# Performance work log

Hardware: AMD Instinct MI355X
Metric: run time of the kernel (lower is better)

## Reference

```python
import jax, jax.numpy as jnp
import numpy as np
import math

SEQLEN, DIM, N_HEADS = 2048, 4096, 32
HEAD_DIM = DIM // N_HEADS
NEG_INF = -1e30  # exp underflows to exactly 0, same effect as -inf without NaN risk


def setup_inputs() -> dict:
    key = jax.random.key(0)
    ks = jax.random.split(key, 7)
    scale = 1.0 / math.sqrt(DIM)
    x = jax.random.normal(ks[0], (SEQLEN, DIM), dtype=jnp.float32)
    weight_q = jax.random.normal(ks[1], (DIM, DIM), dtype=jnp.float32) * scale
    weight_k = jax.random.normal(ks[2], (DIM, DIM), dtype=jnp.float32) * scale
    weight_v = jax.random.normal(ks[3], (DIM, DIM), dtype=jnp.float32) * scale
    weight_o = jax.random.normal(ks[4], (DIM, DIM), dtype=jnp.float32) * scale
    # RoPE frequencies: freqs_cis = exp(i * t * theta_j), standard LLaMA schedule
    inv_freq = 1.0 / (10000.0 ** (np.arange(0, HEAD_DIM, 2, dtype=np.float32) / HEAD_DIM))
    angles = np.arange(SEQLEN, dtype=np.float32)[:, None] * inv_freq[None, :]  # [S, hd/2]
    freqs_cos = jnp.asarray(np.cos(angles), dtype=jnp.float32)
    freqs_sin = jnp.asarray(np.sin(angles), dtype=jnp.float32)
    # additive causal mask [S, S]
    mask = jnp.where(jnp.triu(jnp.ones((SEQLEN, SEQLEN), dtype=bool), k=1), NEG_INF, 0.0).astype(jnp.float32)
    return {"x": x, "weight_q": weight_q, "weight_k": weight_k, "weight_v": weight_v,
            "weight_o": weight_o, "freqs_cos": freqs_cos, "freqs_sin": freqs_sin,
            "mask": mask, "start_pos": 0}


def _apply_rope(t, cos, sin):
    # t: [S, H, hd]; cos/sin: [S, hd/2]
    tr = t.reshape(*t.shape[:-1], -1, 2)           # [S, H, hd/2, 2]
    t_re, t_im = tr[..., 0], tr[..., 1]
    c = cos[:, None, :]
    s = sin[:, None, :]
    out_re = t_re * c - t_im * s
    out_im = t_re * s + t_im * c
    return jnp.stack([out_re, out_im], axis=-1).reshape(t.shape)


def reference(x, weight_q, weight_k, weight_v, weight_o, freqs_cos, freqs_sin, mask, start_pos):
    S, D = x.shape
    hd = freqs_cos.shape[-1] * 2
    H = D // hd
    # the per-head double loop over wq[j][i] is exactly a full [D,D] projection
    xq = (x @ weight_q).reshape(S, H, hd)
    xk = (x @ weight_k).reshape(S, H, hd)
    xv = (x @ weight_v).reshape(S, H, hd)
    xq = _apply_rope(xq, freqs_cos, freqs_sin)
    xk = _apply_rope(xk, freqs_cos, freqs_sin)
    # start_pos == 0 prefill: cache slice == freshly computed keys/values
    scores = jnp.einsum('shd,thd->hst', xq, xk) / jnp.sqrt(jnp.float32(hd))
    scores = scores + mask[None, :, :]
    probs = jax.nn.softmax(scores.astype(jnp.float32), axis=-1).astype(xq.dtype)
    qkv = jnp.einsum('hst,thd->shd', probs, xv).reshape(S, D)
    return qkv @ weight_o
```

## Files before the change

### kernel.cpp

```cpp
#include <hip/hip_runtime.h>
#include <hip/hip_bf16.h>
#include <type_traits>

typedef __hip_bfloat16 bf16;
typedef __attribute__((ext_vector_type(8))) short s8v;
typedef __attribute__((ext_vector_type(4))) short s4v;
typedef __attribute__((ext_vector_type(4))) float f4v;

#define MFMA16(A, B, C) __builtin_amdgcn_mfma_f32_16x16x32_bf16((A), (B), (C), 0, 0, 0)

constexpr int SEQ = 2048;
constexpr int DIM = 4096;
constexpr int NH  = 32;
constexpr int HD  = 128;

__device__ __forceinline__ short f2bs(float f) {
    __hip_bfloat16_raw r = __float2bfloat16(f);
    return (short)r.x;
}

__device__ __forceinline__ void ld_g2l(const bf16* g, bf16* l) {
    __builtin_amdgcn_global_load_lds(
        (const __attribute__((address_space(1))) void*)g,
        (__attribute__((address_space(3))) void*)l, 16, 0, 0);
}

__global__ void convert_bf16(const float* __restrict__ s, bf16* __restrict__ d) {
    int i = blockIdx.x * blockDim.x + threadIdx.x;
    float4 f = ((const float4*)s)[i];
    s4v o;
    o[0] = f2bs(f.x); o[1] = f2bs(f.y); o[2] = f2bs(f.z); o[3] = f2bs(f.w);
    *(s4v*)(d + (size_t)i * 4) = o;
}

__global__ __launch_bounds__(256) void convt_bf16(const float* __restrict__ src,
                                                  bf16* __restrict__ dst,
                                                  int R, int C) {
    __shared__ float t[64][65];
    const int c0 = blockIdx.x * 64, r0 = blockIdx.y * 64;
    const int tid = threadIdx.x;
    const int lr = tid >> 4;
    const int lc = (tid & 15) * 4;
#pragma unroll
    for (int i = 0; i < 4; i++) {
        float4 f = *(const float4*)(src + (size_t)(r0 + lr + 16 * i) * C + c0 + lc);
        t[lr + 16 * i][lc]     = f.x;
        t[lr + 16 * i][lc + 1] = f.y;
        t[lr + 16 * i][lc + 2] = f.z;
        t[lr + 16 * i][lc + 3] = f.w;
    }
    __syncthreads();
    const int oc = tid >> 2;
#pragma unroll
    for (int i = 0; i < 2; i++) {
        int rr = (tid & 3) * 8 + 32 * i;
        s8v o;
#pragma unroll
        for (int e = 0; e < 8; e++) o[e] = f2bs(t[rr + e][oc]);
        *(s8v*)(dst + (size_t)(c0 + oc) * R + r0 + rr) = o;
    }
}

template <typename CT>
__global__ __launch_bounds__(512, 2) void gemm_8p(const bf16* __restrict__ A,
                                                  const bf16* __restrict__ Bt,
                                                  CT* __restrict__ C,
                                                  int M, int N, int K) {
    __shared__ bf16 As_[2][128 * 64];
    __shared__ bf16 Bs_[2][256 * 64];
    const int tid  = threadIdx.x;
    const int lane = tid & 63;
    const int wv   = tid >> 6;
    const int m16  = lane & 15;
    const int quad = lane >> 4;
    const int wm   = wv >> 2, wn = wv & 3;

    const int v   = (int)(blockIdx.y * gridDim.x + blockIdx.x);
    const int s_  = v >> 3;
    const int bn  = (v & 7) * 2 + (s_ >> 4);
    const int bm  = s_ & 15;

    const bf16* Ab = A  + (size_t)bm * 128 * K;
    const bf16* Bb = Bt + (size_t)bn * 256 * K;

    const int i0   = wv * 64 + lane;
    const int row0 = i0 >> 3;
    const int gc8  = ((i0 & 7) ^ (row0 & 7)) * 8;
    const int dst0 = (wv * 64) * 8;
    const int dst1 = (512 + wv * 64) * 8;

    const int aB = (wm * 64 + m16) * 64;
    const int bB = (wn * 64 + m16) * 64;
    const int swz = m16 & 7;
    const int c0k = ((0 + quad) ^ swz) * 8;
    const int c1k = ((4 + quad) ^ swz) * 8;

    const int NT = K >> 6;

    f4v acc[4][4] = {};
    s8v aR[4][2], bR[4][2];

#define STAGEU(gb, lb) do { \
        ld_g2l((gb) + (size_t)row0 * K + gc8, (lb) + dst0); \
        ld_g2l((gb) + (size_t)(row0 + 64) * K + gc8, (lb) + dst1); } while (0)
#define LDA_(i, ks) aR[i][ks] = *(const s8v*)(Ac + aB + (i) * 1024 + ((ks) ? c1k : c0k))
#define LDB_(j, ks) bR[j][ks] = *(const s8v*)(Bc + bB + (j) * 1024 + ((ks) ? c1k : c0k))
#define MMQ(i, j) do { acc[i][j] = MFMA16(aR[i][0], bR[j][0], acc[i][j]); \
                       acc[i][j] = MFMA16(aR[i][1], bR[j][1], acc[i][j]); } while (0)
#define BARX()  __builtin_amdgcn_s_barrier()
#define LGKM0() do { asm volatile("s_waitcnt lgkmcnt(0)" ::: "memory"); \
                     __builtin_amdgcn_sched_barrier(0); } while (0)

    STAGEU(Ab, As_[0]);
    STAGEU(Bb, Bs_[0]);
    STAGEU(Bb + (size_t)128 * K, Bs_[0] + 128 * 64);
    if (NT > 1) {
        STAGEU(Bb + 64, Bs_[1]);
        STAGEU(Bb + (size_t)128 * K + 64, Bs_[1] + 128 * 64);
        STAGEU(Ab + 64, As_[1]);
        asm volatile("s_waitcnt vmcnt(6)" ::: "memory");
    } else {
        asm volatile("s_waitcnt vmcnt(0)" ::: "memory");
    }
    __builtin_amdgcn_sched_barrier(0);
    BARX();

    for (int t = 0; t < NT; ++t) {
        const int cur = t & 1;
        const bf16* Ac = As_[cur];
        const bf16* Bc = Bs_[cur];
        const bool more = (t + 2 < NT);
        const int k2 = (t + 2) << 6;

        LDA_(0, 0); LDA_(0, 1); LDA_(1, 0); LDA_(1, 1);
        LDB_(0, 0); LDB_(0, 1); LDB_(1, 0); LDB_(1, 1);
        BARX(); LGKM0();
        __builtin_amdgcn_s_setprio(1);
        MMQ(0, 0); MMQ(0, 1); MMQ(1, 0); MMQ(1, 1);
        __builtin_amdgcn_s_setprio(0);
        BARX();

        LDB_(2, 0); LDB_(2, 1); LDB_(3, 0); LDB_(3, 1);
        BARX(); LGKM0();
        __builtin_amdgcn_s_setprio(1);
        MMQ(0, 2); MMQ(0, 3); MMQ(1, 2); MMQ(1, 3);
        __builtin_amdgcn_s_setprio(0);
        BARX();

        LDA_(2, 0); LDA_(2, 1); LDA_(3, 0); LDA_(3, 1);
        if (more) {
            STAGEU(Bb + k2, Bs_[cur]);
            STAGEU(Bb + (size_t)128 * K + k2, Bs_[cur] + 128 * 64);
        }
        BARX(); LGKM0();
        __builtin_amdgcn_s_setprio(1);
        MMQ(2, 0); MMQ(2, 1); MMQ(3, 0); MMQ(3, 1);
        __builtin_amdgcn_s_setprio(0);
        BARX();

        if (more) {
            STAGEU(Ab + k2, As_[cur]);
            asm volatile("s_waitcnt vmcnt(6)" ::: "memory");
        } else {
            asm volatile("s_waitcnt vmcnt(0)" ::: "memory");
        }
        __builtin_amdgcn_sched_barrier(0);
        BARX();
        __builtin_amdgcn_s_setprio(1);
        MMQ(2, 2); MMQ(2, 3); MMQ(3, 2); MMQ(3, 3);
        __builtin_amdgcn_s_setprio(0);
        BARX();
    }

#undef STAGEU
#undef LDA_
#undef LDB_
#undef MMQ
#undef BARX
#undef LGKM0

#pragma unroll
    for (int i = 0; i < 4; i++)
#pragma unroll
        for (int j = 0; j < 4; j++)
#pragma unroll
            for (int r = 0; r < 4; r++) {
                int row = bm * 128 + wm * 64 + i * 16 + quad * 4 + r;
                int col = bn * 256 + wn * 64 + j * 16 + m16;
                if constexpr (std::is_same<CT, float>::value)
                    C[(size_t)row * N + col] = acc[i][j][r];
                else
                    C[(size_t)row * N + col] = __float2bfloat16(acc[i][j][r]);
            }
}

template <typename AT, typename CT>
__global__ __launch_bounds__(256) void gemm_nat(const AT* __restrict__ A,
                                                const float* __restrict__ B,
                                                CT* __restrict__ C,
                                                int M, int N, int K) {
    __shared__ short As[128][40];
    __shared__ short Bs[128][40];
    const int tid  = threadIdx.x;
    const int lane = tid & 63;
    const int w    = tid >> 6;
    const int m16  = lane & 15;
    const int quad = lane >> 4;
    const int wm   = w >> 1, wn = w & 1;
    const int bm   = blockIdx.y, bn = blockIdx.x;

    const AT* Ab = A + (size_t)bm * 128 * K;

    f4v acc[4][4] = {};
    const int r0 = tid >> 2;
    const int kc = (tid & 3) * 8;

    for (int k0 = 0; k0 < K; k0 += 32) {
        if constexpr (std::is_same<AT, float>::value) {
#pragma unroll
            for (int half = 0; half < 2; half++) {
                const float* src = Ab + (size_t)(r0 + 64 * half) * K + k0 + kc;
                float4 f0 = *(const float4*)(src);
                float4 f1 = *(const float4*)(src + 4);
                s8v t;
                t[0] = f2bs(f0.x); t[1] = f2bs(f0.y); t[2] = f2bs(f0.z); t[3] = f2bs(f0.w);
                t[4] = f2bs(f1.x); t[5] = f2bs(f1.y); t[6] = f2bs(f1.z); t[7] = f2bs(f1.w);
                *(s8v*)&As[r0 + 64 * half][kc] = t;
            }
        } else {
            *(s8v*)&As[r0][kc]      = *(const s8v*)(Ab + (size_t)r0 * K + k0 + kc);
            *(s8v*)&As[r0 + 64][kc] = *(const s8v*)(Ab + (size_t)(r0 + 64) * K + k0 + kc);
        }
#pragma unroll
        for (int v = tid; v < 512; v += 256) {
            int kr = v >> 4;
            int nc = (v & 15) * 8;
            const float* src = B + (size_t)(k0 + kr) * N + bn * 128 + nc;
            float4 f0 = *(const float4*)(src);
            float4 f1 = *(const float4*)(src + 4);
            Bs[nc + 0][kr] = f2bs(f0.x); Bs[nc + 1][kr] = f2bs(f0.y);
            Bs[nc + 2][kr] = f2bs(f0.z); Bs[nc + 3][kr] = f2bs(f0.w);
            Bs[nc + 4][kr] = f2bs(f1.x); Bs[nc + 5][kr] = f2bs(f1.y);
            Bs[nc + 6][kr] = f2bs(f1.z); Bs[nc + 7][kr] = f2bs(f1.w);
        }
        __syncthreads();

        s8v a[4], b[4];
#pragma unroll
        for (int i = 0; i < 4; i++) a[i] = *(s8v*)&As[wm * 64 + i * 16 + m16][quad * 8];
#pragma unroll
        for (int j = 0; j < 4; j++) b[j] = *(s8v*)&Bs[wn * 64 + j * 16 + m16][quad * 8];
#pragma unroll
        for (int i = 0; i < 4; i++)
#pragma unroll
            for (int j = 0; j < 4; j++) acc[i][j] = MFMA16(a[i], b[j], acc[i][j]);
        __syncthreads();
    }

#pragma unroll
    for (int i = 0; i < 4; i++)
#pragma unroll
        for (int j = 0; j < 4; j++)
#pragma unroll
            for (int r = 0; r < 4; r++) {
                int row = bm * 128 + wm * 64 + i * 16 + quad * 4 + r;
                int col = bn * 128 + wn * 64 + j * 16 + m16;
                if constexpr (std::is_same<CT, float>::value)
                    C[(size_t)row * N + col] = acc[i][j][r];
                else
                    C[(size_t)row * N + col] = __float2bfloat16(acc[i][j][r]);
            }
}

__global__ void rope_kernel(bf16* __restrict__ Q, bf16* __restrict__ K,
                            const float* __restrict__ fc, const float* __restrict__ fs) {
    int tid = blockIdx.x * blockDim.x + threadIdx.x;
    int s = tid >> 11;
    int r = tid & 2047;
    int i = r & 63;
    float c  = fc[s * 64 + i];
    float sn = fs[s * 64 + i];
    size_t idx = (size_t)s * DIM + 2 * r;
    float qre = __bfloat162float(Q[idx]), qim = __bfloat162float(Q[idx + 1]);
    Q[idx]     = __float2bfloat16(qre * c - qim * sn);
    Q[idx + 1] = __float2bfloat16(qre * sn + qim * c);
    float kre = __bfloat162float(K[idx]), kim = __bfloat162float(K[idx + 1]);
    K[idx]     = __float2bfloat16(kre * c - kim * sn);
    K[idx + 1] = __float2bfloat16(kre * sn + kim * c);
}

__global__ __launch_bounds__(256) void attn_kernel(const bf16* __restrict__ Q,
                                                   const bf16* __restrict__ K,
                                                   const bf16* __restrict__ V,
                                                   bf16* __restrict__ O) {
    __shared__ short Ks[64][136];
    __shared__ short Vs[128][72];
    __shared__ short Ps[64][72];

    const int p  = blockIdx.x;
    const int h  = blockIdx.y;
    const int tid  = threadIdx.x;
    const int w    = tid >> 6;
    const int lane = tid & 63;
    const int m16  = lane & 15;
    const int quad = lane >> 4;
    const float scale = 0.08838834764831845f;
    const int NQB = (int)gridDim.x * 2;

    const int rn  = tid >> 4;
    const int rc  = (tid & 15) * 8;
    const int dcs = (tid & 15) & 7;

    for (int half = 0; half < 2; half++) {
        const int qb = half ? (NQB - 1 - p) : p;

        s8v aq[4];
        {
            const bf16* qp = Q + (size_t)(qb * 64 + w * 16 + m16) * DIM + h * HD + quad * 8;
#pragma unroll
            for (int ks = 0; ks < 4; ks++) aq[ks] = *(const s8v*)(qp + ks * 32);
        }

        f4v acc[8] = {};
        float mrow[4] = {-1e30f, -1e30f, -1e30f, -1e30f};
        float lrow[4] = {};

        s8v kreg[4], vreg[4];
        {
            const bf16* kp = K + (size_t)rn * DIM + h * HD + rc;
            const bf16* vp = V + (size_t)rn * DIM + h * HD + rc;
#pragma unroll
            for (int it = 0; it < 4; it++) {
                kreg[it] = *(const s8v*)(kp + (size_t)it * 16 * DIM);
                vreg[it] = *(const s8v*)(vp + (size_t)it * 16 * DIM);
            }
        }

        for (int kt = 0; kt <= qb; kt++) {
#pragma unroll
            for (int it = 0; it < 4; it++)
                *(s8v*)&Ks[it * 16 + rn][rc] = kreg[it];
#pragma unroll
            for (int it = 0; it < 4; it++) {
                int n   = it * 16 + rn;
                int col = (((n >> 3) ^ dcs) << 3) | (n & 7);
#pragma unroll
                for (int e = 0; e < 8; e++) Vs[rc + e][col] = vreg[it][e];
            }
            __syncthreads();

            if (kt < qb) {
                const bf16* kp = K + (size_t)((kt + 1) * 64 + rn) * DIM + h * HD + rc;
                const bf16* vp = V + (size_t)((kt + 1) * 64 + rn) * DIM + h * HD + rc;
#pragma unroll
                for (int it = 0; it < 4; it++) {
                    kreg[it] = *(const s8v*)(kp + (size_t)it * 16 * DIM);
                    vreg[it] = *(const s8v*)(vp + (size_t)it * 16 * DIM);
                }
            }

            f4v sc[4] = {};
#pragma unroll
            for (int j = 0; j < 4; j++)
#pragma unroll
                for (int ks = 0; ks < 4; ks++) {
                    s8v bk = *(s8v*)&Ks[j * 16 + m16][ks * 32 + quad * 8];
                    sc[j] = MFMA16(aq[ks], bk, sc[j]);
                }

            const bool diag = (kt == qb);
#pragma unroll
            for (int j = 0; j < 4; j++)
#pragma unroll
                for (int r = 0; r < 4; r++) {
                    float sv = sc[j][r] * scale;
                    if (diag && (j * 16 + m16) > (w * 16 + quad * 4 + r)) sv = -1e30f;
                    sc[j][r] = sv;
                }

#pragma unroll
            for (int r = 0; r < 4; r++) {
                float mx = fmaxf(fmaxf(sc[0][r], sc[1][r]), fmaxf(sc[2][r], sc[3][r]));
#pragma unroll
                for (int off = 1; off < 16; off <<= 1) mx = fmaxf(mx, __shfl_xor(mx, off, 64));
                float mn    = fmaxf(mrow[r], mx);
                float alpha = __expf(mrow[r] - mn);
                mrow[r] = mn;
                float rs = 0.f;
#pragma unroll
                for (int j = 0; j < 4; j++) {
                    float pj = __expf(sc[j][r] - mn);
                    sc[j][r] = pj;
                    rs += pj;
                }
#pragma unroll
                for (int off = 1; off < 16; off <<= 1) rs += __shfl_xor(rs, off, 64);
                lrow[r] = lrow[r] * alpha + rs;
#pragma unroll
                for (int jo = 0; jo < 8; jo++) acc[jo][r] = acc[jo][r] * alpha;
            }

#pragma unroll
            for (int j = 0; j < 4; j++)
#pragma unroll
                for (int r = 0; r < 4; r++)
                    Ps[w * 16 + quad * 4 + r][j * 16 + m16] = f2bs(sc[j][r]);
            asm volatile("s_waitcnt lgkmcnt(0)" ::: "memory");
            __builtin_amdgcn_sched_barrier(0);

#pragma unroll
            for (int ks2 = 0; ks2 < 2; ks2++) {
                s8v ap = *(s8v*)&Ps[w * 16 + m16][ks2 * 32 + quad * 8];
#pragma unroll
                for (int jo = 0; jo < 8; jo++) {
                    int dv = jo * 16 + m16;
                    int cg = (((ks2 * 4 + quad) ^ ((dv >> 3) & 7)) << 3);
                    s8v bv = *(s8v*)&Vs[dv][cg];
                    acc[jo] = MFMA16(ap, bv, acc[jo]);
                }
            }
            __syncthreads();
        }

#pragma unroll
        for (int jo = 0; jo < 8; jo++)
#pragma unroll
            for (int r = 0; r < 4; r++) {
                float o = acc[jo][r] / fmaxf(lrow[r], 1e-30f);
                int row = qb * 64 + w * 16 + quad * 4 + r;
                int col = h * HD + jo * 16 + m16;
                O[(size_t)row * DIM + col] = __float2bfloat16(o);
            }
    }
}

extern "C" void kernel_launch(void* const* d_in, const int* in_sizes, int n_in,
                              void* d_out, int out_size, void* d_ws, size_t ws_size,
                              hipStream_t stream) {
    const float* x  = (const float*)d_in[0];
    const float* wq = (const float*)d_in[1];
    const float* wk = (const float*)d_in[2];
    const float* wv = (const float*)d_in[3];
    const float* wo = (const float*)d_in[4];
    const float* fc = (const float*)d_in[5];
    const float* fs = (const float*)d_in[6];

    float* out = (float*)d_out;

    const size_t SZ = (size_t)SEQ * DIM;
    const size_t WZ = (size_t)DIM * DIM;
    bf16* Q  = (bf16*)d_ws;
    bf16* Kb = Q + SZ;
    bf16* V  = Kb + SZ;
    bf16* AO = V + SZ;

    const size_t need = (5 * SZ + WZ) * sizeof(bf16);

    if (ws_size >= need) {
        bf16* xb = AO + SZ;
        bf16* wb = xb + SZ;

        dim3 tGw(DIM / 64, DIM / 64);
        dim3 gG8(DIM / 256, SEQ / 128);

        convert_bf16<<<(int)(SZ / 4 / 256), 256, 0, stream>>>(x, xb);

        convt_bf16<<<tGw, 256, 0, stream>>>(wq, wb, DIM, DIM);
        gemm_8p<bf16><<<gG8, 512, 0, stream>>>(xb, wb, Q, SEQ, DIM, DIM);
        convt_bf16<<<tGw, 256, 0, stream>>>(wk, wb, DIM, DIM);
        gemm_8p<bf16><<<gG8, 512, 0, stream>>>(xb, wb, Kb, SEQ, DIM, DIM);
        convt_bf16<<<tGw, 256, 0, stream>>>(wv, wb, DIM, DIM);
        gemm_8p<bf16><<<gG8, 512, 0, stream>>>(xb, wb, V, SEQ, DIM, DIM);

        rope_kernel<<<(SEQ * (DIM / 2)) / 256, 256, 0, stream>>>(Q, Kb, fc, fs);
        attn_kernel<<<dim3(SEQ / 128, NH), 256, 0, stream>>>(Q, Kb, V, AO);

        convt_bf16<<<tGw, 256, 0, stream>>>(wo, wb, DIM, DIM);
        gemm_8p<float><<<gG8, 512, 0, stream>>>(AO, wb, out, SEQ, DIM, DIM);
    } else {
        dim3 gGn(DIM / 128, SEQ / 128);
        gemm_nat<float, bf16><<<gGn, 256, 0, stream>>>(x, wq, Q,  SEQ, DIM, DIM);
        gemm_nat<float, bf16><<<gGn, 256, 0, stream>>>(x, wk, Kb, SEQ, DIM, DIM);
        gemm_nat<float, bf16><<<gGn, 256, 0, stream>>>(x, wv, V,  SEQ, DIM, DIM);
        rope_kernel<<<(SEQ * (DIM / 2)) / 256, 256, 0, stream>>>(Q, Kb, fc, fs);
        attn_kernel<<<dim3(SEQ / 128, NH), 256, 0, stream>>>(Q, Kb, V, AO);
        gemm_nat<bf16, float><<<gGn, 256, 0, stream>>>(AO, wo, out, SEQ, DIM, DIM);
    }
}
```

Before: 752.9 us.

## Use 256x256 GEMM tiles and fuse QKV projections into one launch

The GEMM tile grows from 128x256 to 256x256 per block, doubling the accumulators per wave and raising arithmetic intensity per LDS load. It also stores all three transposed weights side by side in the workspace, so the Q, K and V projections run as one 3*DIM-wide GEMM whose output columns are routed to the separate Q/K/V buffers via a column-block stride. Block swizzling is generalised for arbitrary grid sizes. In exchange the kernel needs more LDS and registers per block, and the fused path needs extra workspace; the output-projection GEMM has only 128 blocks, which may underfill the device.

```diff
diff --git a/kernel.cpp b/kernel.cpp
--- a/kernel.cpp
+++ b/kernel.cpp
@@ -62,11 +62,11 @@
 }
 
 template <typename CT>
-__global__ __launch_bounds__(512, 2) void gemm_8p(const bf16* __restrict__ A,
-                                                  const bf16* __restrict__ Bt,
-                                                  CT* __restrict__ C,
-                                                  int M, int N, int K) {
-    __shared__ bf16 As_[2][128 * 64];
+__global__ __launch_bounds__(512, 2) void gemm_256(const bf16* __restrict__ A,
+                                                   const bf16* __restrict__ Bt,
+                                                   CT* __restrict__ C,
+                                                   int K, size_t cstride) {
+    __shared__ bf16 As_[2][256 * 64];
     __shared__ bf16 Bs_[2][256 * 64];
     const int tid  = threadIdx.x;
     const int lane = tid & 63;
@@ -75,53 +75,49 @@
     const int quad = lane >> 4;
     const int wm   = wv >> 2, wn = wv & 3;
 
-    const int v   = (int)(blockIdx.y * gridDim.x + blockIdx.x);
-    const int s_  = v >> 3;
-    const int bn  = (v & 7) * 2 + (s_ >> 4);
-    const int bm  = s_ & 15;
-
-    const bf16* Ab = A  + (size_t)bm * 128 * K;
+    const int NBN = (int)gridDim.x;
+    const int lin = (int)(blockIdx.y * gridDim.x + blockIdx.x);
+    const int nw8 = (int)(gridDim.x * gridDim.y) >> 3;
+    const int nv  = (lin & 7) * nw8 + (lin >> 3);
+    const int bm  = nv / NBN;
+    const int bn  = nv - bm * NBN;
+
+    const bf16* Ab = A  + (size_t)bm * 256 * K;
     const bf16* Bb = Bt + (size_t)bn * 256 * K;
 
-    const int i0   = wv * 64 + lane;
-    const int row0 = i0 >> 3;
-    const int gc8  = ((i0 & 7) ^ (row0 & 7)) * 8;
-    const int dst0 = (wv * 64) * 8;
-    const int dst1 = (512 + wv * 64) * 8;
-
-    const int aB = (wm * 64 + m16) * 64;
-    const int bB = (wn * 64 + m16) * 64;
+    const int row0 = tid >> 3;
+    const int gc8  = ((tid & 7) ^ (row0 & 7)) * 8;
+    const int dst0 = wv * 512;
+    const int dst1 = 4096 + wv * 512;
+
+    const int aB  = (wm * 128 + m16) * 64;
+    const int bB  = (wn * 64 + m16) * 64;
     const int swz = m16 & 7;
     const int c0k = ((0 + quad) ^ swz) * 8;
     const int c1k = ((4 + quad) ^ swz) * 8;
 
     const int NT = K >> 6;
 
-    f4v acc[4][4] = {};
+    f4v acc[8][4] = {};
     s8v aR[4][2], bR[4][2];
 
-#define STAGEU(gb, lb) do { \
+#define STAGEH(gb, lb) do { \
         ld_g2l((gb) + (size_t)row0 * K + gc8, (lb) + dst0); \
         ld_g2l((gb) + (size_t)(row0 + 64) * K + gc8, (lb) + dst1); } while (0)
-#define LDA_(i, ks) aR[i][ks] = *(const s8v*)(Ac + aB + (i) * 1024 + ((ks) ? c1k : c0k))
-#define LDB_(j, ks) bR[j][ks] = *(const s8v*)(Bc + bB + (j) * 1024 + ((ks) ? c1k : c0k))
-#define MMQ(i, j) do { acc[i][j] = MFMA16(aR[i][0], bR[j][0], acc[i][j]); \
-                       acc[i][j] = MFMA16(aR[i][1], bR[j][1], acc[i][j]); } while (0)
+#define LDA_(i, ks)  aR[i][ks] = *(const s8v*)(Ac + aB + (i) * 1024 + ((ks) ? c1k : c0k))
+#define LDAU_(i, ks) aR[i][ks] = *(const s8v*)(Ac + aB + (i) * 1024 + 4096 + ((ks) ? c1k : c0k))
+#define LDB_(j, ks)  bR[j][ks] = *(const s8v*)(Bc + bB + (j) * 1024 + ((ks) ? c1k : c0k))
+#define MMQ(ai, i, j) do { acc[ai][j] = MFMA16(aR[i][0], bR[j][0], acc[ai][j]); \
+                           acc[ai][j] = MFMA16(aR[i][1], bR[j][1], acc[ai][j]); } while (0)
 #define BARX()  __builtin_amdgcn_s_barrier()
 #define LGKM0() do { asm volatile("s_waitcnt lgkmcnt(0)" ::: "memory"); \
                      __builtin_amdgcn_sched_barrier(0); } while (0)
 
-    STAGEU(Ab, As_[0]);
-    STAGEU(Bb, Bs_[0]);
-    STAGEU(Bb + (size_t)128 * K, Bs_[0] + 128 * 64);
-    if (NT > 1) {
-        STAGEU(Bb + 64, Bs_[1]);
-        STAGEU(Bb + (size_t)128 * K + 64, Bs_[1] + 128 * 64);
-        STAGEU(Ab + 64, As_[1]);
-        asm volatile("s_waitcnt vmcnt(6)" ::: "memory");
-    } else {
-        asm volatile("s_waitcnt vmcnt(0)" ::: "memory");
-    }
+    STAGEH(Ab, As_[0]); STAGEH(Ab + (size_t)128 * K, As_[0] + 8192);
+    STAGEH(Bb, Bs_[0]); STAGEH(Bb + (size_t)128 * K, Bs_[0] + 8192);
+    STAGEH(Ab + 64, As_[1]); STAGEH(Ab + (size_t)128 * K + 64, As_[1] + 8192);
+    STAGEH(Bb + 64, Bs_[1]); STAGEH(Bb + (size_t)128 * K + 64, Bs_[1] + 8192);
+    asm volatile("s_waitcnt vmcnt(8)" ::: "memory");
     __builtin_amdgcn_sched_barrier(0);
     BARX();
 
@@ -133,64 +129,73 @@
         const int k2 = (t + 2) << 6;
 
         LDA_(0, 0); LDA_(0, 1); LDA_(1, 0); LDA_(1, 1);
+        LDA_(2, 0); LDA_(2, 1); LDA_(3, 0); LDA_(3, 1);
         LDB_(0, 0); LDB_(0, 1); LDB_(1, 0); LDB_(1, 1);
         BARX(); LGKM0();
         __builtin_amdgcn_s_setprio(1);
-        MMQ(0, 0); MMQ(0, 1); MMQ(1, 0); MMQ(1, 1);
+        MMQ(0, 0, 0); MMQ(0, 0, 1); MMQ(1, 1, 0); MMQ(1, 1, 1);
+        MMQ(2, 2, 0); MMQ(2, 2, 1); MMQ(3, 3, 0); MMQ(3, 3, 1);
         __builtin_amdgcn_s_setprio(0);
         BARX();
 
         LDB_(2, 0); LDB_(2, 1); LDB_(3, 0); LDB_(3, 1);
         BARX(); LGKM0();
         __builtin_amdgcn_s_setprio(1);
-        MMQ(0, 2); MMQ(0, 3); MMQ(1, 2); MMQ(1, 3);
+        MMQ(0, 0, 2); MMQ(0, 0, 3); MMQ(1, 1, 2); MMQ(1, 1, 3);
+        MMQ(2, 2, 2); MMQ(2, 2, 3); MMQ(3, 3, 2); MMQ(3, 3, 3);
         __builtin_amdgcn_s_setprio(0);
         BARX();
 
-        LDA_(2, 0); LDA_(2, 1); LDA_(3, 0); LDA_(3, 1);
+        LDAU_(0, 0); LDAU_(0, 1); LDAU_(1, 0); LDAU_(1, 1);
+        LDAU_(2, 0); LDAU_(2, 1); LDAU_(3, 0); LDAU_(3, 1);
         if (more) {
-            STAGEU(Bb + k2, Bs_[cur]);
-            STAGEU(Bb + (size_t)128 * K + k2, Bs_[cur] + 128 * 64);
+            STAGEH(Bb + k2, Bs_[cur]);
+            STAGEH(Bb + (size_t)128 * K + k2, Bs_[cur] + 8192);
         }
         BARX(); LGKM0();
         __builtin_amdgcn_s_setprio(1);
-        MMQ(2, 0); MMQ(2, 1); MMQ(3, 0); MMQ(3, 1);
+        MMQ(4, 0, 0); MMQ(4, 0, 1); MMQ(5, 1, 0); MMQ(5, 1, 1);
+        MMQ(6, 2, 0); MMQ(6, 2, 1); MMQ(7, 3, 0); MMQ(7, 3, 1);
         __builtin_amdgcn_s_setprio(0);
         BARX();
 
         if (more) {
-            STAGEU(Ab + k2, As_[cur]);
-            asm volatile("s_waitcnt vmcnt(6)" ::: "memory");
+            STAGEH(Ab + k2, As_[cur]);
+            STAGEH(Ab + (size_t)128 * K + k2, As_[cur] + 8192);
+            asm volatile("s_waitcnt vmcnt(8)" ::: "memory");
         } else {
             asm volatile("s_waitcnt vmcnt(0)" ::: "memory");
         }
         __builtin_amdgcn_sched_barrier(0);
         BARX();
         __builtin_amdgcn_s_setprio(1);
-        MMQ(2, 2); MMQ(2, 3); MMQ(3, 2); MMQ(3, 3);
+        MMQ(4, 0, 2); MMQ(4, 0, 3); MMQ(5, 1, 2); MMQ(5, 1, 3);
+        MMQ(6, 2, 2); MMQ(6, 2, 3); MMQ(7, 3, 2); MMQ(7, 3, 3);
         __builtin_amdgcn_s_setprio(0);
         BARX();
     }
 
-#undef STAGEU
+#undef STAGEH
 #undef LDA_
+#undef LDAU_
 #undef LDB_
 #undef MMQ
 #undef BARX
 #undef LGKM0
 
 #pragma unroll
-    for (int i = 0; i < 4; i++)
+    for (int i = 0; i < 8; i++)
 #pragma unroll
         for (int j = 0; j < 4; j++)
 #pragma unroll
             for (int r = 0; r < 4; r++) {
-                int row = bm * 128 + wm * 64 + i * 16 + quad * 4 + r;
-                int col = bn * 256 + wn * 64 + j * 16 + m16;
+                int row = bm * 256 + wm * 128 + i * 16 + quad * 4 + r;
+                int ct  = bn * 256 + wn * 64 + j * 16 + m16;
+                CT* dst = C + (size_t)(ct >> 12) * cstride + (size_t)row * DIM + (ct & 4095);
                 if constexpr (std::is_same<CT, float>::value)
-                    C[(size_t)row * N + col] = acc[i][j][r];
+                    *dst = acc[i][j][r];
                 else
-                    C[(size_t)row * N + col] = __float2bfloat16(acc[i][j][r]);
+                    *dst = __float2bfloat16(acc[i][j][r]);
             }
 }
 
@@ -454,29 +459,49 @@
     bf16* V  = Kb + SZ;
     bf16* AO = V + SZ;
 
-    const size_t need = (5 * SZ + WZ) * sizeof(bf16);
-
-    if (ws_size >= need) {
+    const size_t needF = (5 * SZ + 3 * WZ) * sizeof(bf16);
+    const size_t needU = (5 * SZ + WZ) * sizeof(bf16);
+
+    dim3 tGw(DIM / 64, DIM / 64);
+
+    if (ws_size >= needF) {
         bf16* xb = AO + SZ;
         bf16* wb = xb + SZ;
 
-        dim3 tGw(DIM / 64, DIM / 64);
-        dim3 gG8(DIM / 256, SEQ / 128);
-
         convert_bf16<<<(int)(SZ / 4 / 256), 256, 0, stream>>>(x, xb);
-
         convt_bf16<<<tGw, 256, 0, stream>>>(wq, wb, DIM, DIM);
-        gemm_8p<bf16><<<gG8, 512, 0, stream>>>(xb, wb, Q, SEQ, DIM, DIM);
-        convt_bf16<<<tGw, 256, 0, stream>>>(wk, wb, DIM, DIM);
-        gemm_8p<bf16><<<gG8, 512, 0, stream>>>(xb, wb, Kb, SEQ, DIM, DIM);
-        convt_bf16<<<tGw, 256, 0, stream>>>(wv, wb, DIM, DIM);
-        gemm_8p<bf16><<<gG8, 512, 0, stream>>>(xb, wb, V, SEQ, DIM, DIM);
+        convt_bf16<<<tGw, 256, 0, stream>>>(wk, wb + WZ, DIM, DIM);
+        convt_bf16<<<tGw, 256, 0, stream>>>(wv, wb + 2 * WZ, DIM, DIM);
+
+        gemm_256<bf16><<<dim3(3 * DIM / 256, SEQ / 256), 512, 0, stream>>>(
+            xb, wb, Q, DIM, SZ);
 
         rope_kernel<<<(SEQ * (DIM / 2)) / 256, 256, 0, stream>>>(Q, Kb, fc, fs);
         attn_kernel<<<dim3(SEQ / 128, NH), 256, 0, stream>>>(Q, Kb, V, AO);
 
         convt_bf16<<<tGw, 256, 0, stream>>>(wo, wb, DIM, DIM);
-        gemm_8p<float><<<gG8, 512, 0, stream>>>(AO, wb, out, SEQ, DIM, DIM);
+        gemm_256<float><<<dim3(DIM / 256, SEQ / 256), 512, 0, stream>>>(
+            AO, wb, out, DIM, 0);
+    } else if (ws_size >= needU) {
+        bf16* xb = AO + SZ;
+        bf16* wb = xb + SZ;
+
+        dim3 gU(DIM / 256, SEQ / 256);
+
+        convert_bf16<<<(int)(SZ / 4 / 256), 256, 0, stream>>>(x, xb);
+
+        convt_bf16<<<tGw, 256, 0, stream>>>(wq, wb, DIM, DIM);
+        gemm_256<bf16><<<gU, 512, 0, stream>>>(xb, wb, Q, DIM, 0);
+        convt_bf16<<<tGw, 256, 0, stream>>>(wk, wb, DIM, DIM);
+        gemm_256<bf16><<<gU, 512, 0, stream>>>(xb, wb, Kb, DIM, 0);
+        convt_bf16<<<tGw, 256, 0, stream>>>(wv, wb, DIM, DIM);
+        gemm_256<bf16><<<gU, 512, 0, stream>>>(xb, wb, V, DIM, 0);
+
+        rope_kernel<<<(SEQ * (DIM / 2)) / 256, 256, 0, stream>>>(Q, Kb, fc, fs);
+        attn_kernel<<<dim3(SEQ / 128, NH), 256, 0, stream>>>(Q, Kb, V, AO);
+
+        convt_bf16<<<tGw, 256, 0, stream>>>(wo, wb, DIM, DIM);
+        gemm_256<float><<<gU, 512, 0, stream>>>(AO, wb, out, DIM, 0);
     } else {
         dim3 gGn(DIM / 128, SEQ / 128);
         gemm_nat<float, bf16><<<gGn, 256, 0, stream>>>(x, wq, Q,  SEQ, DIM, DIM);
```

After: 822.0 us. +9.2%, slower.
